# Performance work log

Measured on AMD Instinct MI355X. Metric: run time of the kernel, lower is better.

The kernel has to match this reference:

```python
import jax, jax.numpy as jnp
import numpy as np

TAU = 0.2
VTH = 0.3


def setup_inputs() -> dict:
    key = jax.random.key(0)
    x = jax.random.normal(key, (32, 128, 32, 32, 8), dtype=jnp.float32)
    return {"x": x}


def reference(x):
    # x: [B, C, H, W, T]; LIF membrane update scanned over time (last axis).
    xt = jnp.moveaxis(x, -1, 0)  # [T, B, C, H, W]
    u0 = jnp.zeros(x.shape[:-1], dtype=x.dtype)
    o0 = jnp.zeros(x.shape[:-1], dtype=x.dtype)

    def step(carry, x_t):
        u_prev, o_prev = carry
        u = TAU * u_prev * (1.0 - o_prev) + x_t
        o = (u - VTH > 0).astype(x_t.dtype)  # hard threshold spike
        return (u, o), o

    _, out_t = jax.lax.scan(step, (u0, o0), xt)
    return jnp.moveaxis(out_t, 0, -1)  # [B, C, H, W, T]
```

## Files before the change

### kernel.cpp

```cpp
#include <hip/hip_runtime.h>

#define TAU 0.2f
#define VTH 0.3f

__global__ __launch_bounds__(256) void LIFSpike_73864847556979_kernel(
    const float* __restrict__ x, float* __restrict__ out, int n_pixels) {
    int idx = blockIdx.x * blockDim.x + threadIdx.x;
    if (idx >= n_pixels) return;

    const float4* __restrict__ xp = (const float4*)(x + (size_t)idx * 8);
    float4 a = xp[0];
    float4 b = xp[1];

    float v[8] = {a.x, a.y, a.z, a.w, b.x, b.y, b.z, b.w};
    float r[8];

    float u = 0.0f;
    float o = 0.0f;
#pragma unroll
    for (int t = 0; t < 8; ++t) {
        u = TAU * u * (1.0f - o) + v[t];
        o = (u - VTH > 0.0f) ? 1.0f : 0.0f;
        r[t] = o;
    }

    float4* __restrict__ op = (float4*)(out + (size_t)idx * 8);
    op[0] = make_float4(r[0], r[1], r[2], r[3]);
    op[1] = make_float4(r[4], r[5], r[6], r[7]);
}

extern "C" void kernel_launch(void* const* d_in, const int* in_sizes, int n_in,
                              void* d_out, int out_size, void* d_ws, size_t ws_size,
                              hipStream_t stream) {
    const float* x = (const float*)d_in[0];
    float* out = (float*)d_out;
    int n_pixels = in_sizes[0] / 8;
    int block = 256;
    int grid = (n_pixels + block - 1) / block;
    LIFSpike_73864847556979_kernel<<<grid, block, 0, stream>>>(x, out, n_pixels);
}
```

Baseline: 227.2 us.

## Stage tiles through padded LDS for coalesced loads and nontemporal stores

Each block loads its 256-pixel tile as fully coalesced float4 accesses, with consecutive threads touching consecutive 16-byte chunks. It transposes the tile through padded shared memory so each thread gets its own 8 timesteps, then writes the spikes back through LDS and stores them coalesced with nontemporal hints. This replaces the strided two-float4-per-thread access pattern. The cost is two barriers and LDS traffic, and the bounds check is dropped on the assumption that the pixel count is a multiple of 256.

```diff
diff --git a/kernel.cpp b/kernel.cpp
--- a/kernel.cpp
+++ b/kernel.cpp
@@ -3,30 +3,46 @@
 #define TAU 0.2f
 #define VTH 0.3f
 
+#define PPB 256
+#define PADF 12
+
+typedef float v4f __attribute__((ext_vector_type(4)));
+
 __global__ __launch_bounds__(256) void LIFSpike_73864847556979_kernel(
-    const float* __restrict__ x, float* __restrict__ out, int n_pixels) {
-    int idx = blockIdx.x * blockDim.x + threadIdx.x;
-    if (idx >= n_pixels) return;
+    const float* __restrict__ x, float* __restrict__ out) {
+    __shared__ float lds[PPB * PADF];
+    const int t = threadIdx.x;
+    const size_t base_f4 = (size_t)blockIdx.x * (PPB * 2);
 
-    const float4* __restrict__ xp = (const float4*)(x + (size_t)idx * 8);
-    float4 a = xp[0];
-    float4 b = xp[1];
+    const v4f* __restrict__ xin = (const v4f*)x + base_f4;
+    v4f* __restrict__ xout = (v4f*)out + base_f4;
 
-    float v[8] = {a.x, a.y, a.z, a.w, b.x, b.y, b.z, b.w};
+    v4f a = xin[t];
+    v4f b = xin[t + 256];
+    const int j0 = t, j1 = t + 256;
+    *(v4f*)&lds[(j0 >> 1) * PADF + (j0 & 1) * 4] = a;
+    *(v4f*)&lds[(j1 >> 1) * PADF + (j1 & 1) * 4] = b;
+    __syncthreads();
+
+    v4f lo = *(const v4f*)&lds[t * PADF];
+    v4f hi = *(const v4f*)&lds[t * PADF + 4];
+    float v[8] = {lo.x, lo.y, lo.z, lo.w, hi.x, hi.y, hi.z, hi.w};
     float r[8];
+    float u = 0.0f, o = 0.0f;
+#pragma unroll
+    for (int k = 0; k < 8; ++k) {
+        u = TAU * u * (1.0f - o) + v[k];
+        o = (u > VTH) ? 1.0f : 0.0f;
+        r[k] = o;
+    }
+    *(v4f*)&lds[t * PADF] = (v4f){r[0], r[1], r[2], r[3]};
+    *(v4f*)&lds[t * PADF + 4] = (v4f){r[4], r[5], r[6], r[7]};
+    __syncthreads();
 
-    float u = 0.0f;
-    float o = 0.0f;
-#pragma unroll
-    for (int t = 0; t < 8; ++t) {
-        u = TAU * u * (1.0f - o) + v[t];
-        o = (u - VTH > 0.0f) ? 1.0f : 0.0f;
-        r[t] = o;
-    }
-
-    float4* __restrict__ op = (float4*)(out + (size_t)idx * 8);
-    op[0] = make_float4(r[0], r[1], r[2], r[3]);
-    op[1] = make_float4(r[4], r[5], r[6], r[7]);
+    v4f c = *(const v4f*)&lds[(j0 >> 1) * PADF + (j0 & 1) * 4];
+    v4f d = *(const v4f*)&lds[(j1 >> 1) * PADF + (j1 & 1) * 4];
+    __builtin_nontemporal_store(c, &xout[t]);
+    __builtin_nontemporal_store(d, &xout[t + 256]);
 }
 
 extern "C" void kernel_launch(void* const* d_in, const int* in_sizes, int n_in,
@@ -35,7 +51,6 @@
     const float* x = (const float*)d_in[0];
     float* out = (float*)d_out;
     int n_pixels = in_sizes[0] / 8;
-    int block = 256;
-    int grid = (n_pixels + block - 1) / block;
-    LIFSpike_73864847556979_kernel<<<grid, block, 0, stream>>>(x, out, n_pixels);
+    int grid = n_pixels / PPB;
+    LIFSpike_73864847556979_kernel<<<grid, PPB, 0, stream>>>(x, out);
 }
```

Result: no change. 227.9 us (+0.3%).
